# Optimization experiments

Hardware: AMD Instinct MI355X
Metric: run time of the kernel (lower is better)

## Reference

```python
import jax, jax.numpy as jnp
import numpy as np

NUM_USERS = 100000
NUM_ITEMS = 100000
D = 64          # embed_dim
B = 4096        # batch of users (rows of sparse interaction matrix)
NNZ = 204800    # nonzeros in sparse user-item matrix (~50 items/user)
N = 1048576     # number of (user,item) pairs to score
DROPOUT = 0.2


def setup_inputs() -> dict:
    key = jax.random.key(0)
    ks = jax.random.split(key, 10)
    return {
        "user_ids": jax.random.randint(ks[0], (B,), 0, NUM_USERS, dtype=jnp.int32),
        "bat_idx": jax.random.randint(ks[1], (N,), 0, B, dtype=jnp.int32),
        "sp_row": jax.random.randint(ks[2], (NNZ,), 0, B, dtype=jnp.int32),
        "sp_col": jax.random.randint(ks[3], (NNZ,), 0, NUM_ITEMS, dtype=jnp.int32),
        "bat_items": jax.random.randint(ks[4], (N,), 0, NUM_ITEMS, dtype=jnp.int32),
        # learned parameters (normal init for embeddings, zeros for offset/bias, as in reset_parameters)
        "en_emb": jax.random.normal(ks[5], (NUM_ITEMS, D), dtype=jnp.float32) * 0.01,
        "en_offset": jnp.zeros((D,), dtype=jnp.float32),
        "de_emb": jax.random.normal(ks[6], (NUM_ITEMS, D), dtype=jnp.float32) * 0.01,
        "de_bias": jnp.zeros((NUM_ITEMS,), dtype=jnp.float32),
        "user_emb": jax.random.normal(ks[7], (NUM_USERS, D), dtype=jnp.float32) * 0.01,
    }


def reference(user_ids, bat_idx, sp_row, sp_col, bat_items,
              en_emb, en_offset, de_emb, de_bias, user_emb):
    keep = 1.0 - DROPOUT
    # dropout_sparse: bernoulli keep-mask on sparse nnz values (binary 1.0), rescaled by 1/keep
    drop_mask = jax.random.bernoulli(jax.random.key(42), keep, (NNZ,))
    vals = drop_mask.astype(en_emb.dtype) / keep  # corrupted sparse values [NNZ]

    # sparse @ dense: sum_j A[b,j] * en_emb[j]  ->  gather + segment_sum  -> [B, D]
    hidden = jax.ops.segment_sum(vals[:, None] * en_emb[sp_col], sp_row, num_segments=B)
    hidden = jnp.tanh(hidden + user_emb[user_ids] + en_offset[None, :])

    # decode: inner product of gathered hidden rows and item embeddings
    h = hidden[bat_idx]                      # [N, D]
    de_i = de_emb[bat_items]                 # [N, D]
    ratings = jnp.sum(h * de_i, axis=-1) + de_bias[bat_items]  # [N]

    # l2 reg over unique bat_items rows (mask-based == torch.unique gather)
    item_mask = jnp.zeros((NUM_ITEMS,), en_emb.dtype).at[bat_items].set(1.0)
    reg_loss = 0.5 * (
        jnp.sum(item_mask * jnp.sum(en_emb ** 2, axis=-1))
        + jnp.sum(en_offset ** 2)
        + jnp.sum(user_emb[user_ids] ** 2)
        + jnp.sum(item_mask * jnp.sum(de_emb ** 2, axis=-1))
        + jnp.sum(item_mask * de_bias ** 2)
    )
    return ratings, reg_loss
```

## Files before the change

### kernel.cpp

```cpp
#include <hip/hip_runtime.h>
#include <hip/hip_bf16.h>

#define PARTITIONABLE 1
#define NB 8
#define CAPB 136192
#define FATB 2048
#define CAPR 128
#define RSB 200
#define SCVT 1024
#define HBLK 1024
#define REGF 64
#define REGB_FB 256

__device__ __forceinline__ unsigned rotl32(unsigned x, int r) {
    return (x << r) | (x >> (32 - r));
}

__device__ __forceinline__ void threefry2x32(unsigned k0, unsigned k1,
                                             unsigned& x0, unsigned& x1) {
    unsigned ks0 = k0, ks1 = k1, ks2 = k0 ^ k1 ^ 0x1BD11BDAu;
    x0 += ks0; x1 += ks1;
#define TF_R(r) { x0 += x1; x1 = rotl32(x1, r); x1 ^= x0; }
    TF_R(13) TF_R(15) TF_R(26) TF_R(6)   x0 += ks1; x1 += ks2 + 1u;
    TF_R(17) TF_R(29) TF_R(16) TF_R(24)  x0 += ks2; x1 += ks0 + 2u;
    TF_R(13) TF_R(15) TF_R(26) TF_R(6)   x0 += ks0; x1 += ks1 + 3u;
    TF_R(17) TF_R(29) TF_R(16) TF_R(24)  x0 += ks1; x1 += ks2 + 4u;
    TF_R(13) TF_R(15) TF_R(26) TF_R(6)   x0 += ks2; x1 += ks0 + 5u;
#undef TF_R
}

__device__ __forceinline__ bool keep_mask(int i, int nnz) {
#if PARTITIONABLE
    unsigned x0 = 0u, x1 = (unsigned)i;
    threefry2x32(0u, 42u, x0, x1);
    unsigned bits = x0 ^ x1;
#else
    int half = nnz >> 1;
    int j = (i < half) ? i : i - half;
    unsigned x0 = (unsigned)j, x1 = (unsigned)(j + half);
    threefry2x32(0u, 42u, x0, x1);
    unsigned bits = (i < half) ? x0 : x1;
#endif
    float u = __uint_as_float((bits >> 9) | 0x3f800000u) - 1.0f;
    return u < 0.8f;
}

__device__ __forceinline__ unsigned short f2bf(float f) {
    unsigned u = __float_as_uint(f);
    return (unsigned short)((u + 0x7FFFu + ((u >> 16) & 1u)) >> 16);
}

__device__ __forceinline__ float bfdot8(uint4 h, uint4 d) {
    float s;
    s  = __uint_as_float(h.x << 16)         * __uint_as_float(d.x << 16);
    s += __uint_as_float(h.x & 0xFFFF0000u) * __uint_as_float(d.x & 0xFFFF0000u);
    s += __uint_as_float(h.y << 16)         * __uint_as_float(d.y << 16);
    s += __uint_as_float(h.y & 0xFFFF0000u) * __uint_as_float(d.y & 0xFFFF0000u);
    s += __uint_as_float(h.z << 16)         * __uint_as_float(d.z << 16);
    s += __uint_as_float(h.z & 0xFFFF0000u) * __uint_as_float(d.z & 0xFFFF0000u);
    s += __uint_as_float(h.w << 16)         * __uint_as_float(d.w << 16);
    s += __uint_as_float(h.w & 0xFFFF0000u) * __uint_as_float(d.w & 0xFFFF0000u);
    return s;
}

__global__ void k_prep(const int* __restrict__ bat_idx, const int* __restrict__ bat_items,
                       unsigned char* __restrict__ mask, int* __restrict__ cursor,
                       uint2* __restrict__ perm2,
                       const int* __restrict__ sp_row, const int* __restrict__ sp_col,
                       int* __restrict__ rowcur, unsigned* __restrict__ srow,
                       const float* __restrict__ en_emb, const float* __restrict__ de_emb,
                       const float* __restrict__ de_bias, const float* __restrict__ user_emb,
                       const int* __restrict__ user_ids, const float* __restrict__ en_off,
                       unsigned short* __restrict__ debf, float* __restrict__ sq,
                       float* __restrict__ reg_ws,
                       int N, int num_items, int nnz, int B) {
    __shared__ int sh[4096];
    if (blockIdx.x < 256) {
        if (threadIdx.x < NB) sh[threadIdx.x] = 0;
        __syncthreads();
        const int per = N / 256;
        const int base_n = blockIdx.x * per;
        const int iters = per / blockDim.x;
        unsigned packed[16];
        int bkt[16];
        for (int it = 0; it < iters; ++it) {
            int n = base_n + it * blockDim.x + threadIdx.x;
            int item = bat_items[n];
            int bidx = bat_idx[n];
            mask[item] = 1;
            int b = (int)(((unsigned long long)(unsigned)item * NB) / (unsigned)num_items);
            packed[it] = ((unsigned)item << 12) | (unsigned)bidx;
            bkt[it] = b;
            atomicAdd(&sh[b], 1);
        }
        __syncthreads();
        if (threadIdx.x < NB) {
            int c = sh[threadIdx.x];
            sh[threadIdx.x] = atomicAdd(&cursor[threadIdx.x], c);
        }
        __syncthreads();
        for (int it = 0; it < iters; ++it) {
            int n = base_n + it * blockDim.x + threadIdx.x;
            int pos = atomicAdd(&sh[bkt[it]], 1);
            unsigned gpos = (unsigned)bkt[it] * CAPB + (unsigned)min(pos, CAPB - 1);
            perm2[gpos] = make_uint2(packed[it], (unsigned)n);
        }
    } else if (blockIdx.x < 256 + RSB) {
        const int blk = blockIdx.x - 256;
        for (int i = threadIdx.x; i < B; i += blockDim.x) sh[i] = 0;
        __syncthreads();
        const int per = nnz / RSB;
        const int base = blk * per;
        const int iters = per / blockDim.x;
        unsigned pk[8];
        int rw[8];
        for (int it = 0; it < iters; ++it) {
            int i = base + it * blockDim.x + threadIdx.x;
            int row = sp_row[i];
            int col = sp_col[i];
            bool k = keep_mask(i, nnz);
            pk[it] = (unsigned)col;
            rw[it] = k ? row : -1;
            if (k) atomicAdd(&sh[row], 1);
        }
        __syncthreads();
        for (int i = threadIdx.x; i < B; i += blockDim.x) {
            int c = sh[i];
            if (c) sh[i] = atomicAdd(&rowcur[i], c);
        }
        __syncthreads();
        for (int it = 0; it < iters; ++it) {
            if (rw[it] >= 0) {
                int pos = atomicAdd(&sh[rw[it]], 1);
                srow[(size_t)rw[it] * CAPR + min(pos, CAPR - 1)] = pk[it];
            }
        }
    } else {
        const int bx = blockIdx.x - (256 + RSB);
        const int stride = SCVT * blockDim.x;
        for (int t = bx * blockDim.x + threadIdx.x; t < num_items * 16; t += stride) {
            int i = t >> 4, l = t & 15;
            float4 d = *reinterpret_cast<const float4*>(de_emb + (size_t)i * 64 + l * 4);
            float4 e = *reinterpret_cast<const float4*>(en_emb + (size_t)i * 64 + l * 4);
            ushort4 o;
            o.x = f2bf(d.x); o.y = f2bf(d.y); o.z = f2bf(d.z); o.w = f2bf(d.w);
            reinterpret_cast<ushort4*>(debf)[t] = o;
            float q = e.x*e.x + e.y*e.y + e.z*e.z + e.w*e.w
                    + d.x*d.x + d.y*d.y + d.z*d.z + d.w*d.w;
            if (l == 0) { float bb = de_bias[i]; q += bb * bb; }
            q += __shfl_xor(q, 1);
            q += __shfl_xor(q, 2);
            q += __shfl_xor(q, 4);
            q += __shfl_xor(q, 8);
            if (l == 0) sq[i] = q;
        }
        float s = 0.f;
        for (int t = bx * blockDim.x + threadIdx.x; t < B * 16; t += stride) {
            int b = t >> 4, l = t & 15;
            int uid = user_ids[b];
            float4 u = *reinterpret_cast<const float4*>(user_emb + (size_t)uid * 64 + l * 4);
            s += u.x*u.x + u.y*u.y + u.z*u.z + u.w*u.w;
        }
        if (bx == 0 && threadIdx.x < 64) {
            float o = en_off[threadIdx.x];
            s += o * o;
        }
        for (int m = 1; m < 64; m <<= 1) s += __shfl_xor(s, m);
        float* wsum = (float*)sh;
        if ((threadIdx.x & 63) == 0) wsum[threadIdx.x >> 6] = s;
        __syncthreads();
        if (threadIdx.x == 0)
            atomicAdd(reg_ws, wsum[0] + wsum[1] + wsum[2] + wsum[3]);
    }
}

__global__ void k_hidden_reg(const unsigned* __restrict__ srow, const int* __restrict__ rowcur,
                             const float* __restrict__ en_emb, const float* __restrict__ user_emb,
                             const int* __restrict__ user_ids, const float* __restrict__ en_off,
                             unsigned short* __restrict__ hb,
                             const unsigned char* __restrict__ mask,
                             const float* __restrict__ sq,
                             float* __restrict__ reg_ws, int B, int num_items) {
    if (blockIdx.x < HBLK) {
        const int lane = threadIdx.x & 63;
        const int row = (blockIdx.x * blockDim.x + threadIdx.x) >> 6;
        if (row >= B) return;
        const int cnt = min(rowcur[row], CAPR);
        const unsigned* sr = srow + (size_t)row * CAPR;
        float acc0 = 0.f, acc1 = 0.f, acc2 = 0.f, acc3 = 0.f;
        float acc4 = 0.f, acc5 = 0.f, acc6 = 0.f, acc7 = 0.f;
        for (int j0 = 0; j0 < cnt; j0 += 64) {
            unsigned ev = (j0 + lane < cnt) ? sr[j0 + lane] : 0u;
            int m = min(64, cnt - j0);
            int jj = 0;
            for (; jj + 7 < m; jj += 8) {
                unsigned e0 = __shfl(ev, jj);
                unsigned e1 = __shfl(ev, jj + 1);
                unsigned e2 = __shfl(ev, jj + 2);
                unsigned e3 = __shfl(ev, jj + 3);
                unsigned e4 = __shfl(ev, jj + 4);
                unsigned e5 = __shfl(ev, jj + 5);
                unsigned e6 = __shfl(ev, jj + 6);
                unsigned e7 = __shfl(ev, jj + 7);
                acc0 += en_emb[(size_t)e0 * 64 + lane];
                acc1 += en_emb[(size_t)e1 * 64 + lane];
                acc2 += en_emb[(size_t)e2 * 64 + lane];
                acc3 += en_emb[(size_t)e3 * 64 + lane];
                acc4 += en_emb[(size_t)e4 * 64 + lane];
                acc5 += en_emb[(size_t)e5 * 64 + lane];
                acc6 += en_emb[(size_t)e6 * 64 + lane];
                acc7 += en_emb[(size_t)e7 * 64 + lane];
            }
            for (; jj + 3 < m; jj += 4) {
                unsigned e0 = __shfl(ev, jj);
                unsigned e1 = __shfl(ev, jj + 1);
                unsigned e2 = __shfl(ev, jj + 2);
                unsigned e3 = __shfl(ev, jj + 3);
                acc0 += en_emb[(size_t)e0 * 64 + lane];
                acc1 += en_emb[(size_t)e1 * 64 + lane];
                acc2 += en_emb[(size_t)e2 * 64 + lane];
                acc3 += en_emb[(size_t)e3 * 64 + lane];
            }
            for (; jj < m; ++jj) {
                unsigned e0 = __shfl(ev, jj);
                acc0 += en_emb[(size_t)e0 * 64 + lane];
            }
        }
        int uid = user_ids[row];
        float hval = 1.25f * (((acc0 + acc1) + (acc2 + acc3))
                            + ((acc4 + acc5) + (acc6 + acc7)))
                   + user_emb[(size_t)uid * 64 + lane] + en_off[lane];
        hb[(size_t)row * 64 + lane] = f2bf(tanhf(hval));
    } else {
        const int bx = blockIdx.x - HBLK;
        const int stride = REGF * blockDim.x;
        float s = 0.f;
        for (int i = bx * blockDim.x + threadIdx.x; i < num_items; i += stride)
            s += (float)mask[i] * sq[i];
        for (int m = 1; m < 64; m <<= 1) s += __shfl_xor(s, m);
        __shared__ float wsum[4];
        if ((threadIdx.x & 63) == 0) wsum[threadIdx.x >> 6] = s;
        __syncthreads();
        if (threadIdx.x == 0)
            atomicAdd(reg_ws, wsum[0] + wsum[1] + wsum[2] + wsum[3]);
    }
}

__global__ void k_ratings_bkt(const unsigned short* __restrict__ hb,
                              const unsigned short* __restrict__ debf,
                              const float* __restrict__ de_bias,
                              const uint2* __restrict__ perm2, const int* __restrict__ cursor,
                              const float* __restrict__ reg_ws,
                              float* __restrict__ out, int N) {
    if (blockIdx.x == 0 && threadIdx.x == 0)
        out[N] = 0.5f * reg_ws[0];
    const int bkt = blockIdx.x & (NB - 1);
    const int cnt = cursor[bkt];
    const int l = threadIdx.x & 7;
    const int gid = (blockIdx.x >> 3) * (blockDim.x >> 3) + (threadIdx.x >> 3);
    const int gpb = (gridDim.x >> 3) * (blockDim.x >> 3);
    const uint2* pb = perm2 + (size_t)bkt * CAPB;

    int slot = gid;
    for (; slot + 3 * gpb < cnt; slot += 4 * gpb) {
        uint2 p0 = pb[slot];
        uint2 p1 = pb[slot + gpb];
        uint2 p2 = pb[slot + 2 * gpb];
        uint2 p3 = pb[slot + 3 * gpb];
        int it0 = (int)(p0.x >> 12), b0 = (int)(p0.x & 0xFFFu);
        int it1 = (int)(p1.x >> 12), b1 = (int)(p1.x & 0xFFFu);
        int it2 = (int)(p2.x >> 12), b2 = (int)(p2.x & 0xFFFu);
        int it3 = (int)(p3.x >> 12), b3 = (int)(p3.x & 0xFFFu);
        uint4 h0 = *reinterpret_cast<const uint4*>(hb   + (size_t)b0  * 64 + l * 8);
        uint4 d0 = *reinterpret_cast<const uint4*>(debf + (size_t)it0 * 64 + l * 8);
        uint4 h1 = *reinterpret_cast<const uint4*>(hb   + (size_t)b1  * 64 + l * 8);
        uint4 d1 = *reinterpret_cast<const uint4*>(debf + (size_t)it1 * 64 + l * 8);
        uint4 h2 = *reinterpret_cast<const uint4*>(hb   + (size_t)b2  * 64 + l * 8);
        uint4 d2 = *reinterpret_cast<const uint4*>(debf + (size_t)it2 * 64 + l * 8);
        uint4 h3 = *reinterpret_cast<const uint4*>(hb   + (size_t)b3  * 64 + l * 8);
        uint4 d3 = *reinterpret_cast<const uint4*>(debf + (size_t)it3 * 64 + l * 8);
        float s0 = bfdot8(h0, d0);
        float s1 = bfdot8(h1, d1);
        float s2 = bfdot8(h2, d2);
        float s3 = bfdot8(h3, d3);
        s0 += __shfl_xor(s0, 1); s1 += __shfl_xor(s1, 1);
        s2 += __shfl_xor(s2, 1); s3 += __shfl_xor(s3, 1);
        s0 += __shfl_xor(s0, 2); s1 += __shfl_xor(s1, 2);
        s2 += __shfl_xor(s2, 2); s3 += __shfl_xor(s3, 2);
        s0 += __shfl_xor(s0, 4); s1 += __shfl_xor(s1, 4);
        s2 += __shfl_xor(s2, 4); s3 += __shfl_xor(s3, 4);
        if (l == 0) {
            out[p0.y] = s0 + de_bias[it0];
            out[p1.y] = s1 + de_bias[it1];
            out[p2.y] = s2 + de_bias[it2];
            out[p3.y] = s3 + de_bias[it3];
        }
    }
    for (; slot < cnt; slot += gpb) {
        uint2 p = pb[slot];
        int item = (int)(p.x >> 12), bidx = (int)(p.x & 0xFFFu);
        uint4 hv = *reinterpret_cast<const uint4*>(hb   + (size_t)bidx * 64 + l * 8);
        uint4 dv = *reinterpret_cast<const uint4*>(debf + (size_t)item * 64 + l * 8);
        float s = bfdot8(hv, dv);
        s += __shfl_xor(s, 1);
        s += __shfl_xor(s, 2);
        s += __shfl_xor(s, 4);
        if (l == 0) out[p.y] = s + de_bias[item];
    }
}

__global__ void k_mask(const int* __restrict__ bat_items, unsigned char* __restrict__ mask,
                       int N) {
    int t = blockIdx.x * blockDim.x + threadIdx.x;
    if (t < N) mask[bat_items[t]] = 1;
}

__global__ void k_ratings(const float* __restrict__ hidden, const float* __restrict__ de_emb,
                          const float* __restrict__ de_bias,
                          const int* __restrict__ bat_idx, const int* __restrict__ bat_items,
                          float* __restrict__ out, int N) {
    const int l = threadIdx.x & 15;
    const int gid = (blockIdx.x * blockDim.x + threadIdx.x) >> 4;
    const int gstride = (gridDim.x * blockDim.x) >> 4;
    for (int n = gid; n < N; n += gstride) {
        int b  = bat_idx[n];
        int it = bat_items[n];
        float4 hv = *reinterpret_cast<const float4*>(hidden + (size_t)b  * 64 + l * 4);
        float4 dv = *reinterpret_cast<const float4*>(de_emb + (size_t)it * 64 + l * 4);
        float s = hv.x*dv.x + hv.y*dv.y + hv.z*dv.z + hv.w*dv.w;
        s += __shfl_xor(s, 1);
        s += __shfl_xor(s, 2);
        s += __shfl_xor(s, 4);
        s += __shfl_xor(s, 8);
        if (l == 0) out[n] = s + de_bias[it];
    }
}

__global__ void k_scatter(const int* __restrict__ sp_row, const int* __restrict__ sp_col,
                          const float* __restrict__ en_emb, float* __restrict__ hidden,
                          int nnz) {
    const int lane = threadIdx.x & 63;
    const int wave = (blockIdx.x * blockDim.x + threadIdx.x) >> 6;
    const int nwaves = (gridDim.x * blockDim.x) >> 6;
    for (int i = wave; i < nnz; i += nwaves) {
        if (!keep_mask(i, nnz)) continue;
        int row = sp_row[i];
        int col = sp_col[i];
        float v = 1.25f * en_emb[(size_t)col * 64 + lane];
        atomicAdd(&hidden[row * 64 + lane], v);
    }
}

__global__ void k_hfinish(float* __restrict__ hidden, const float* __restrict__ user_emb,
                          const int* __restrict__ user_ids, const float* __restrict__ en_off,
                          int B) {
    int t = blockIdx.x * blockDim.x + threadIdx.x;
    if (t >= B * 64) return;
    int b = t >> 6, d = t & 63;
    int uid = user_ids[b];
    float h = hidden[t] + user_emb[(size_t)uid * 64 + d] + en_off[d];
    hidden[t] = tanhf(h);
}

__global__ void k_reg_fb(const unsigned char* __restrict__ mask,
                         const float* __restrict__ en_emb, const float* __restrict__ de_emb,
                         const float* __restrict__ de_bias,
                         const float* __restrict__ user_emb, const int* __restrict__ user_ids,
                         const float* __restrict__ en_off,
                         float* __restrict__ reg, int num_items, int B) {
    const int stride = gridDim.x * blockDim.x;
    float s = 0.f;
    for (int t = blockIdx.x * blockDim.x + threadIdx.x; t < num_items * 16; t += stride) {
        int i = t >> 4, l = t & 15;
        if (mask[i]) {
            float4 e = *reinterpret_cast<const float4*>(en_emb + (size_t)i * 64 + l * 4);
            float4 d = *reinterpret_cast<const float4*>(de_emb + (size_t)i * 64 + l * 4);
            s += e.x*e.x + e.y*e.y + e.z*e.z + e.w*e.w
               + d.x*d.x + d.y*d.y + d.z*d.z + d.w*d.w;
            if (l == 0) { float bb = de_bias[i]; s += bb * bb; }
        }
    }
    for (int t = blockIdx.x * blockDim.x + threadIdx.x; t < B * 16; t += stride) {
        int b = t >> 4, l = t & 15;
        int uid = user_ids[b];
        float4 u = *reinterpret_cast<const float4*>(user_emb + (size_t)uid * 64 + l * 4);
        s += u.x*u.x + u.y*u.y + u.z*u.z + u.w*u.w;
    }
    if (blockIdx.x == 0 && threadIdx.x < 64) {
        float o = en_off[threadIdx.x];
        s += o * o;
    }
    for (int m = 1; m < 64; m <<= 1) s += __shfl_xor(s, m);
    __shared__ float wsum[4];
    if ((threadIdx.x & 63) == 0) wsum[threadIdx.x >> 6] = s;
    __syncthreads();
    if (threadIdx.x == 0)
        atomicAdd(reg, 0.5f * (wsum[0] + wsum[1] + wsum[2] + wsum[3]));
}

extern "C" void kernel_launch(void* const* d_in, const int* in_sizes, int n_in,
                              void* d_out, int out_size, void* d_ws, size_t ws_size,
                              hipStream_t stream) {
    const int*   user_ids  = (const int*)  d_in[0];
    const int*   bat_idx   = (const int*)  d_in[1];
    const int*   sp_row    = (const int*)  d_in[2];
    const int*   sp_col    = (const int*)  d_in[3];
    const int*   bat_items = (const int*)  d_in[4];
    const float* en_emb    = (const float*)d_in[5];
    const float* en_off    = (const float*)d_in[6];
    const float* de_emb    = (const float*)d_in[7];
    const float* de_bias   = (const float*)d_in[8];
    const float* user_emb  = (const float*)d_in[9];

    const int B         = in_sizes[0];
    const int N         = in_sizes[1];
    const int NNZ       = in_sizes[2];
    const int NUM_ITEMS = in_sizes[8];

    float* out = (float*)d_out;

    char* ws = (char*)d_ws;
    size_t off = 0;
    unsigned char* mask = (unsigned char*)(ws + off);
    off += ((size_t)NUM_ITEMS + 255) & ~(size_t)255;
    int* cursor = (int*)(ws + off);               off += 256;
    int* rowcur = (int*)(ws + off);               off += (size_t)B * 4;
    float* reg_ws = (float*)(ws + off);           off += 256;
    const size_t zero_bytes = off;
    float* hidden = (float*)(ws + off);           off += (size_t)B * 64 * 4;
    off = (off + 15) & ~(size_t)15;
    uint2* perm2 = (uint2*)(ws + off);            off += (size_t)NB * CAPB * 8;
    unsigned* srow = (unsigned*)(ws + off);       off += (size_t)B * CAPR * 4;
    unsigned short* hb   = (unsigned short*)(ws + off);  off += (size_t)B * 64 * 2;
    off = (off + 15) & ~(size_t)15;
    unsigned short* debf = (unsigned short*)(ws + off);  off += (size_t)NUM_ITEMS * 64 * 2;
    float* sq = (float*)(ws + off);                      off += (size_t)NUM_ITEMS * 4;

    const bool sorted_path =
        (ws_size >= off) && (N == (1 << 20)) && (B == 4096) &&
        (NUM_ITEMS <= (1 << 17)) && (NUM_ITEMS >= 65536) &&
        (NUM_ITEMS % 4 == 0) &&
        (NNZ % (RSB * 256) == 0) && (NNZ / RSB <= CAPR * 256);

    hipMemsetAsync(ws, 0, zero_bytes, stream);

    if (sorted_path) {
        k_prep<<<256 + RSB + SCVT, 256, 0, stream>>>(
            bat_idx, bat_items, mask, cursor, perm2,
            sp_row, sp_col, rowcur, srow,
            en_emb, de_emb, de_bias, user_emb, user_ids, en_off,
            debf, sq, reg_ws, N, NUM_ITEMS, NNZ, B);
        k_hidden_reg<<<HBLK + REGF, 256, 0, stream>>>(
            srow, rowcur, en_emb, user_emb, user_ids, en_off, hb,
            mask, sq, reg_ws, B, NUM_ITEMS);
        k_ratings_bkt<<<FATB, 256, 0, stream>>>(hb, debf, de_bias, perm2, cursor,
                                                reg_ws, out, N);
    } else {
        hipMemsetAsync(hidden, 0, (size_t)B * 64 * 4, stream);
        hipMemsetAsync(out + N, 0, sizeof(float), stream);
        k_mask<<<(N + 255) / 256, 256, 0, stream>>>(bat_items, mask, N);
        k_scatter<<<FATB, 256, 0, stream>>>(sp_row, sp_col, en_emb, hidden, NNZ);
        k_hfinish<<<(B * 64 + 255) / 256, 256, 0, stream>>>(hidden, user_emb, user_ids,
                                                            en_off, B);
        k_ratings<<<FATB, 256, 0, stream>>>(hidden, de_emb, de_bias, bat_idx, bat_items, out, N);
        k_reg_fb<<<REGB_FB, 256, 0, stream>>>(mask, en_emb, de_emb, de_bias,
                                              user_emb, user_ids, en_off, out + N, NUM_ITEMS, B);
    }
}
```

Measured before the change: 175.5 us.

## Rebalance work across three kernels to overlap sort, bucketing and conversion

Work is redistributed across the three launches. The sparse-row sort and half of the embedding bf16 conversion go in the first kernel. The hidden computation runs alongside the pair bucketing and the second half of the conversion in the middle kernel. The masked reg reduction moves into the ratings kernel, which uses a completion counter to write the final loss. The intent is to balance work between launches so latency-bound phases overlap with bandwidth-heavy streaming, at the cost of a threadfence/atomic handshake and extra blocks in the ratings launch.

```diff
diff --git a/kernel.cpp b/kernel.cpp
--- a/kernel.cpp
+++ b/kernel.cpp
@@ -7,7 +7,9 @@
 #define FATB 2048
 #define CAPR 128
 #define RSB 200
-#define SCVT 1024
+#define SA 512
+#define SB 512
+#define TS (SA + SB)
 #define HBLK 1024
 #define REGF 64
 #define REGB_FB 256
@@ -63,50 +65,40 @@
     return s;
 }
 
-__global__ void k_prep(const int* __restrict__ bat_idx, const int* __restrict__ bat_items,
-                       unsigned char* __restrict__ mask, int* __restrict__ cursor,
-                       uint2* __restrict__ perm2,
-                       const int* __restrict__ sp_row, const int* __restrict__ sp_col,
+__device__ __forceinline__ void stream_body(int j, int num_items,
+                                            const float* __restrict__ en_emb,
+                                            const float* __restrict__ de_emb,
+                                            const float* __restrict__ de_bias,
+                                            unsigned short* __restrict__ debf,
+                                            float* __restrict__ sq) {
+    const int stride = TS * 256;
+    for (int t = j * 256 + threadIdx.x; t < num_items * 16; t += stride) {
+        int i = t >> 4, l = t & 15;
+        float4 d = *reinterpret_cast<const float4*>(de_emb + (size_t)i * 64 + l * 4);
+        float4 e = *reinterpret_cast<const float4*>(en_emb + (size_t)i * 64 + l * 4);
+        ushort4 o;
+        o.x = f2bf(d.x); o.y = f2bf(d.y); o.z = f2bf(d.z); o.w = f2bf(d.w);
+        reinterpret_cast<ushort4*>(debf)[t] = o;
+        float q = e.x*e.x + e.y*e.y + e.z*e.z + e.w*e.w
+                + d.x*d.x + d.y*d.y + d.z*d.z + d.w*d.w;
+        if (l == 0) { float bb = de_bias[i]; q += bb * bb; }
+        q += __shfl_xor(q, 1);
+        q += __shfl_xor(q, 2);
+        q += __shfl_xor(q, 4);
+        q += __shfl_xor(q, 8);
+        if (l == 0) sq[i] = q;
+    }
+}
+
+__global__ void k_sort(const int* __restrict__ sp_row, const int* __restrict__ sp_col,
                        int* __restrict__ rowcur, unsigned* __restrict__ srow,
                        const float* __restrict__ en_emb, const float* __restrict__ de_emb,
-                       const float* __restrict__ de_bias, const float* __restrict__ user_emb,
-                       const int* __restrict__ user_ids, const float* __restrict__ en_off,
+                       const float* __restrict__ de_bias,
                        unsigned short* __restrict__ debf, float* __restrict__ sq,
-                       float* __restrict__ reg_ws,
-                       int N, int num_items, int nnz, int B) {
+                       int num_items, int nnz, int B) {
     __shared__ int sh[4096];
-    if (blockIdx.x < 256) {
-        if (threadIdx.x < NB) sh[threadIdx.x] = 0;
-        __syncthreads();
-        const int per = N / 256;
-        const int base_n = blockIdx.x * per;
-        const int iters = per / blockDim.x;
-        unsigned packed[16];
-        int bkt[16];
-        for (int it = 0; it < iters; ++it) {
-            int n = base_n + it * blockDim.x + threadIdx.x;
-            int item = bat_items[n];
-            int bidx = bat_idx[n];
-            mask[item] = 1;
-            int b = (int)(((unsigned long long)(unsigned)item * NB) / (unsigned)num_items);
-            packed[it] = ((unsigned)item << 12) | (unsigned)bidx;
-            bkt[it] = b;
-            atomicAdd(&sh[b], 1);
-        }
-        __syncthreads();
-        if (threadIdx.x < NB) {
-            int c = sh[threadIdx.x];
-            sh[threadIdx.x] = atomicAdd(&cursor[threadIdx.x], c);
-        }
-        __syncthreads();
-        for (int it = 0; it < iters; ++it) {
-            int n = base_n + it * blockDim.x + threadIdx.x;
-            int pos = atomicAdd(&sh[bkt[it]], 1);
-            unsigned gpos = (unsigned)bkt[it] * CAPB + (unsigned)min(pos, CAPB - 1);
-            perm2[gpos] = make_uint2(packed[it], (unsigned)n);
-        }
-    } else if (blockIdx.x < 256 + RSB) {
-        const int blk = blockIdx.x - 256;
+    if (blockIdx.x < RSB) {
+        const int blk = blockIdx.x;
         for (int i = threadIdx.x; i < B; i += blockDim.x) sh[i] = 0;
         __syncthreads();
         const int per = nnz / RSB;
@@ -136,51 +128,22 @@
             }
         }
     } else {
-        const int bx = blockIdx.x - (256 + RSB);
-        const int stride = SCVT * blockDim.x;
-        for (int t = bx * blockDim.x + threadIdx.x; t < num_items * 16; t += stride) {
-            int i = t >> 4, l = t & 15;
-            float4 d = *reinterpret_cast<const float4*>(de_emb + (size_t)i * 64 + l * 4);
-            float4 e = *reinterpret_cast<const float4*>(en_emb + (size_t)i * 64 + l * 4);
-            ushort4 o;
-            o.x = f2bf(d.x); o.y = f2bf(d.y); o.z = f2bf(d.z); o.w = f2bf(d.w);
-            reinterpret_cast<ushort4*>(debf)[t] = o;
-            float q = e.x*e.x + e.y*e.y + e.z*e.z + e.w*e.w
-                    + d.x*d.x + d.y*d.y + d.z*d.z + d.w*d.w;
-            if (l == 0) { float bb = de_bias[i]; q += bb * bb; }
-            q += __shfl_xor(q, 1);
-            q += __shfl_xor(q, 2);
-            q += __shfl_xor(q, 4);
-            q += __shfl_xor(q, 8);
-            if (l == 0) sq[i] = q;
-        }
-        float s = 0.f;
-        for (int t = bx * blockDim.x + threadIdx.x; t < B * 16; t += stride) {
-            int b = t >> 4, l = t & 15;
-            int uid = user_ids[b];
-            float4 u = *reinterpret_cast<const float4*>(user_emb + (size_t)uid * 64 + l * 4);
-            s += u.x*u.x + u.y*u.y + u.z*u.z + u.w*u.w;
-        }
-        if (bx == 0 && threadIdx.x < 64) {
-            float o = en_off[threadIdx.x];
-            s += o * o;
-        }
-        for (int m = 1; m < 64; m <<= 1) s += __shfl_xor(s, m);
-        float* wsum = (float*)sh;
-        if ((threadIdx.x & 63) == 0) wsum[threadIdx.x >> 6] = s;
-        __syncthreads();
-        if (threadIdx.x == 0)
-            atomicAdd(reg_ws, wsum[0] + wsum[1] + wsum[2] + wsum[3]);
-    }
-}
-
-__global__ void k_hidden_reg(const unsigned* __restrict__ srow, const int* __restrict__ rowcur,
-                             const float* __restrict__ en_emb, const float* __restrict__ user_emb,
-                             const int* __restrict__ user_ids, const float* __restrict__ en_off,
-                             unsigned short* __restrict__ hb,
-                             const unsigned char* __restrict__ mask,
-                             const float* __restrict__ sq,
-                             float* __restrict__ reg_ws, int B, int num_items) {
+        stream_body(blockIdx.x - RSB, num_items, en_emb, de_emb, de_bias, debf, sq);
+    }
+}
+
+__global__ void k_mid(const unsigned* __restrict__ srow, const int* __restrict__ rowcur,
+                      const float* __restrict__ en_emb, const float* __restrict__ user_emb,
+                      const int* __restrict__ user_ids, const float* __restrict__ en_off,
+                      unsigned short* __restrict__ hb,
+                      const int* __restrict__ bat_idx, const int* __restrict__ bat_items,
+                      unsigned char* __restrict__ mask, int* __restrict__ cursor,
+                      uint2* __restrict__ perm2,
+                      const float* __restrict__ de_emb, const float* __restrict__ de_bias,
+                      unsigned short* __restrict__ debf, float* __restrict__ sq,
+                      float* __restrict__ reg_ws,
+                      int N, int num_items, int B) {
+    __shared__ int sh[64];
     if (blockIdx.x < HBLK) {
         const int lane = threadIdx.x & 63;
         const int row = (blockIdx.x * blockDim.x + threadIdx.x) >> 6;
@@ -231,34 +194,93 @@
                             + ((acc4 + acc5) + (acc6 + acc7)))
                    + user_emb[(size_t)uid * 64 + lane] + en_off[lane];
         hb[(size_t)row * 64 + lane] = f2bf(tanhf(hval));
+    } else if (blockIdx.x < HBLK + 256) {
+        const int bb = blockIdx.x - HBLK;
+        if (threadIdx.x < NB) sh[threadIdx.x] = 0;
+        __syncthreads();
+        const int per = N / 256;
+        const int base_n = bb * per;
+        const int iters = per / blockDim.x;
+        unsigned packed[16];
+        int bkt[16];
+        for (int it = 0; it < iters; ++it) {
+            int n = base_n + it * blockDim.x + threadIdx.x;
+            int item = bat_items[n];
+            int bidx = bat_idx[n];
+            mask[item] = 1;
+            int b = (int)(((unsigned long long)(unsigned)item * NB) / (unsigned)num_items);
+            packed[it] = ((unsigned)item << 12) | (unsigned)bidx;
+            bkt[it] = b;
+            atomicAdd(&sh[b], 1);
+        }
+        __syncthreads();
+        if (threadIdx.x < NB) {
+            int c = sh[threadIdx.x];
+            sh[threadIdx.x] = atomicAdd(&cursor[threadIdx.x], c);
+        }
+        __syncthreads();
+        for (int it = 0; it < iters; ++it) {
+            int n = base_n + it * blockDim.x + threadIdx.x;
+            int pos = atomicAdd(&sh[bkt[it]], 1);
+            unsigned gpos = (unsigned)bkt[it] * CAPB + (unsigned)min(pos, CAPB - 1);
+            perm2[gpos] = make_uint2(packed[it], (unsigned)n);
+        }
     } else {
-        const int bx = blockIdx.x - HBLK;
+        const int j2 = blockIdx.x - (HBLK + 256);
+        stream_body(SA + j2, num_items, en_emb, de_emb, de_bias, debf, sq);
+        float s = 0.f;
+        const int stride2 = SB * 256;
+        for (int t = j2 * 256 + threadIdx.x; t < B * 16; t += stride2) {
+            int b = t >> 4, l = t & 15;
+            int uid = user_ids[b];
+            float4 u = *reinterpret_cast<const float4*>(user_emb + (size_t)uid * 64 + l * 4);
+            s += u.x*u.x + u.y*u.y + u.z*u.z + u.w*u.w;
+        }
+        if (j2 == 0 && threadIdx.x < 64) {
+            float o = en_off[threadIdx.x];
+            s += o * o;
+        }
+        for (int m = 1; m < 64; m <<= 1) s += __shfl_xor(s, m);
+        float* wsum = (float*)sh;
+        if ((threadIdx.x & 63) == 0) wsum[threadIdx.x >> 6] = s;
+        __syncthreads();
+        if (threadIdx.x == 0)
+            atomicAdd(reg_ws, wsum[0] + wsum[1] + wsum[2] + wsum[3]);
+    }
+}
+
+__global__ void k_ratings_bkt(const unsigned short* __restrict__ hb,
+                              const unsigned short* __restrict__ debf,
+                              const float* __restrict__ de_bias,
+                              const uint2* __restrict__ perm2, const int* __restrict__ cursor,
+                              const unsigned char* __restrict__ mask,
+                              const float* __restrict__ sq,
+                              float* __restrict__ reg_ws, int* __restrict__ done_cnt,
+                              float* __restrict__ out, int N, int num_items) {
+    if (blockIdx.x < REGF) {
         const int stride = REGF * blockDim.x;
         float s = 0.f;
-        for (int i = bx * blockDim.x + threadIdx.x; i < num_items; i += stride)
+        for (int i = blockIdx.x * blockDim.x + threadIdx.x; i < num_items; i += stride)
             s += (float)mask[i] * sq[i];
         for (int m = 1; m < 64; m <<= 1) s += __shfl_xor(s, m);
         __shared__ float wsum[4];
         if ((threadIdx.x & 63) == 0) wsum[threadIdx.x >> 6] = s;
         __syncthreads();
-        if (threadIdx.x == 0)
+        if (threadIdx.x == 0) {
             atomicAdd(reg_ws, wsum[0] + wsum[1] + wsum[2] + wsum[3]);
-    }
-}
-
-__global__ void k_ratings_bkt(const unsigned short* __restrict__ hb,
-                              const unsigned short* __restrict__ debf,
-                              const float* __restrict__ de_bias,
-                              const uint2* __restrict__ perm2, const int* __restrict__ cursor,
-                              const float* __restrict__ reg_ws,
-                              float* __restrict__ out, int N) {
-    if (blockIdx.x == 0 && threadIdx.x == 0)
-        out[N] = 0.5f * reg_ws[0];
-    const int bkt = blockIdx.x & (NB - 1);
+            __threadfence();
+            int old = atomicAdd(done_cnt, 1);
+            if (old == REGF - 1)
+                out[N] = 0.5f * atomicAdd(reg_ws, 0.0f);
+        }
+        return;
+    }
+    const int bid = blockIdx.x - REGF;
+    const int bkt = bid & (NB - 1);
     const int cnt = cursor[bkt];
     const int l = threadIdx.x & 7;
-    const int gid = (blockIdx.x >> 3) * (blockDim.x >> 3) + (threadIdx.x >> 3);
-    const int gpb = (gridDim.x >> 3) * (blockDim.x >> 3);
+    const int gid = (bid >> 3) * (blockDim.x >> 3) + (threadIdx.x >> 3);
+    const int gpb = ((gridDim.x - REGF) >> 3) * (blockDim.x >> 3);
     const uint2* pb = perm2 + (size_t)bkt * CAPB;
 
     int slot = gid;
@@ -425,7 +447,8 @@
     off += ((size_t)NUM_ITEMS + 255) & ~(size_t)255;
     int* cursor = (int*)(ws + off);               off += 256;
     int* rowcur = (int*)(ws + off);               off += (size_t)B * 4;
-    float* reg_ws = (float*)(ws + off);           off += 256;
+    float* reg_ws = (float*)(ws + off);
+    int* done_cnt = (int*)(ws + off) + 1;         off += 256;
     const size_t zero_bytes = off;
     float* hidden = (float*)(ws + off);           off += (size_t)B * 64 * 4;
     off = (off + 15) & ~(size_t)15;
@@ -445,16 +468,16 @@
     hipMemsetAsync(ws, 0, zero_bytes, stream);
 
     if (sorted_path) {
-        k_prep<<<256 + RSB + SCVT, 256, 0, stream>>>(
+        k_sort<<<RSB + SA, 256, 0, stream>>>(
+            sp_row, sp_col, rowcur, srow,
+            en_emb, de_emb, de_bias, debf, sq, NUM_ITEMS, NNZ, B);
+        k_mid<<<HBLK + 256 + SB, 256, 0, stream>>>(
+            srow, rowcur, en_emb, user_emb, user_ids, en_off, hb,
             bat_idx, bat_items, mask, cursor, perm2,
-            sp_row, sp_col, rowcur, srow,
-            en_emb, de_emb, de_bias, user_emb, user_ids, en_off,
-            debf, sq, reg_ws, N, NUM_ITEMS, NNZ, B);
-        k_hidden_reg<<<HBLK + REGF, 256, 0, stream>>>(
-            srow, rowcur, en_emb, user_emb, user_ids, en_off, hb,
-            mask, sq, reg_ws, B, NUM_ITEMS);
-        k_ratings_bkt<<<FATB, 256, 0, stream>>>(hb, debf, de_bias, perm2, cursor,
-                                                reg_ws, out, N);
+            de_emb, de_bias, debf, sq, reg_ws, N, NUM_ITEMS, B);
+        k_ratings_bkt<<<REGF + FATB, 256, 0, stream>>>(
+            hb, debf, de_bias, perm2, cursor, mask, sq,
+            reg_ws, done_cnt, out, N, NUM_ITEMS);
     } else {
         hipMemsetAsync(hidden, 0, (size_t)B * 64 * 4, stream);
         hipMemsetAsync(out + N, 0, sizeof(float), stream);
```

Result: no change. 178.8 us (+1.9%).
